# Optimization experiments

Hardware: AMD Instinct MI355X
Metric: run time of the kernel (lower is better)

## Reference

```python
import jax, jax.numpy as jnp
import numpy as np

N_NODES, N_EDGES, D, H, G = 50000, 800000, 128, 128, 2048
EPS_BN = 1e-5


def _bn(x, g, b, m, v):
    # inference-mode BatchNorm1d
    return (x - m) * jax.lax.rsqrt(v + EPS_BN) * g + b


def _gin_mlp(h, w1, b1, g1, be1, m1, v1, w2, b2, g2, be2, m2, v2):
    h = jax.nn.relu(_bn(h @ w1 + b1, g1, be1, m1, v1))
    return jax.nn.relu(_bn(h @ w2 + b2, g2, be2, m2, v2))


def _gin(x, src, dst, *mlp_params):
    # GINConv with eps=0: MLP(x_i + sum_{j->i} x_j)
    agg = jax.ops.segment_sum(x[src], dst, num_segments=x.shape[0])
    return _gin_mlp(x + agg, *mlp_params)


def setup_inputs() -> dict:
    key = jax.random.key(0)
    ks = jax.random.split(key, 16)
    inp = {
        'x': jax.random.normal(ks[0], (N_NODES, D), dtype=jnp.float32),
        'edge_index': jax.random.randint(ks[1], (2, N_EDGES), 0, N_NODES, dtype=jnp.int64),
        'batch': jnp.sort(jax.random.randint(ks[2], (N_NODES,), 0, G, dtype=jnp.int64)),
    }
    def lin(k, fin, fout):
        return jax.random.normal(k, (fin, fout), dtype=jnp.float32) * (1.0 / np.sqrt(fin))
    # conv1 MLP
    inp.update(w11=lin(ks[3], D, H), b11=jnp.zeros((H,)), g11=jnp.ones((H,)), be11=jnp.zeros((H,)), m11=jnp.zeros((H,)), v11=jnp.ones((H,)))
    inp.update(w12=lin(ks[4], H, H), b12=jnp.zeros((H,)), g12=jnp.ones((H,)), be12=jnp.zeros((H,)), m12=jnp.zeros((H,)), v12=jnp.ones((H,)))
    # conv2 MLP
    inp.update(w21=lin(ks[5], H, H), b21=jnp.zeros((H,)), g21=jnp.ones((H,)), be21=jnp.zeros((H,)), m21=jnp.zeros((H,)), v21=jnp.ones((H,)))
    inp.update(w22=lin(ks[6], H, H), b22=jnp.zeros((H,)), g22=jnp.ones((H,)), be22=jnp.zeros((H,)), m22=jnp.zeros((H,)), v22=jnp.ones((H,)))
    # classifier
    inp.update(wc1=lin(ks[7], H, 64), bc1=jnp.zeros((64,)), gc1=jnp.ones((64,)), bec1=jnp.zeros((64,)), mc1=jnp.zeros((64,)), vc1=jnp.ones((64,)))
    inp.update(wc2=lin(ks[8], 64, 2), bc2=jnp.zeros((2,)))
    return inp


def reference(x, edge_index, batch,
              w11, b11, g11, be11, m11, v11, w12, b12, g12, be12, m12, v12,
              w21, b21, g21, be21, m21, v21, w22, b22, g22, be22, m22, v22,
              wc1, bc1, gc1, bec1, mc1, vc1, wc2, bc2):
    src, dst = edge_index[0], edge_index[1]
    out1 = _gin(x, src, dst, w11, b11, g11, be11, m11, v11, w12, b12, g12, be12, m12, v12)
    # F.relu on already-ReLU'd output is a no-op but kept for fidelity
    out1 = jax.nn.relu(out1)
    out2 = _gin(out1, src, dst, w21, b21, g21, be21, m21, v21, w22, b22, g22, be22, m22, v22)
    out2 = jax.nn.relu(out2)
    # global mean pool over graph ids
    sums = jax.ops.segment_sum(out2, batch, num_segments=G)
    cnt = jax.ops.segment_sum(jnp.ones((out2.shape[0],), out2.dtype), batch, num_segments=G)
    pooled = sums / jnp.maximum(cnt, 1.0)[:, None]
    # classifier (dropout = identity in eval)
    h = jax.nn.relu(_bn(pooled @ wc1 + bc1, gc1, bec1, mc1, vc1))
    logits = h @ wc2 + bc2
    return logits
```

## Files before the change

kernel.cpp:

```cpp
#include <hip/hip_runtime.h>

#define NN 50000
#define NE 800000
#define DD 128
#define GG 2048
#define EPS 1e-5f
#define NBUK 196
#define CHUNK 4096
#define CAP 5120
#define CVTB 3125

typedef __attribute__((ext_vector_type(8))) short short8;
typedef __attribute__((ext_vector_type(4))) float floatx4;

__device__ __forceinline__ ushort f2b(float f) {
  uint u = __float_as_uint(f);
  uint r = ((u >> 16) & 1u) + 0x7fffu;
  return (ushort)((u + r) >> 16);
}
__device__ __forceinline__ float b2f(ushort h) {
  return __uint_as_float(((uint)h) << 16);
}
__device__ __forceinline__ float blo(uint u) { return __uint_as_float(u << 16); }
__device__ __forceinline__ float bhi(uint u) { return __uint_as_float(u & 0xffff0000u); }

__global__ __launch_bounds__(256) void k_pre(
    const float* __restrict__ W11, const float* __restrict__ W12,
    const float* __restrict__ W21, const float* __restrict__ W22,
    const float* __restrict__ b11, const float* __restrict__ g11,
    const float* __restrict__ be11, const float* __restrict__ m11,
    const float* __restrict__ v11,
    const float* __restrict__ b12, const float* __restrict__ g12,
    const float* __restrict__ be12, const float* __restrict__ m12,
    const float* __restrict__ v12,
    const float* __restrict__ b21, const float* __restrict__ g21,
    const float* __restrict__ be21, const float* __restrict__ m21,
    const float* __restrict__ v21,
    const float* __restrict__ b22, const float* __restrict__ g22,
    const float* __restrict__ be22, const float* __restrict__ m22,
    const float* __restrict__ v22,
    ushort* __restrict__ Wb, float* __restrict__ albb,
    int* __restrict__ buk_cnt) {
  int t = threadIdx.x;
  int b = blockIdx.x;
  if (b == 64) {
    buk_cnt[t] = 0;
    if (t < DD) {
      float a;
      a = g11[t] * rsqrtf(v11[t] + EPS);
      albb[0 * DD + t] = a;
      albb[1 * DD + t] = (b11[t] - m11[t]) * a + be11[t];
      a = g12[t] * rsqrtf(v12[t] + EPS);
      albb[2 * DD + t] = a;
      albb[3 * DD + t] = (b12[t] - m12[t]) * a + be12[t];
      a = g21[t] * rsqrtf(v21[t] + EPS);
      albb[4 * DD + t] = a;
      albb[5 * DD + t] = (b21[t] - m21[t]) * a + be21[t];
      a = g22[t] * rsqrtf(v22[t] + EPS);
      albb[6 * DD + t] = a;
      albb[7 * DD + t] = (b22[t] - m22[t]) * a + be22[t];
    }
    return;
  }
  const float* Ws[4] = {W11, W12, W21, W22};
  int widx = b >> 4;
  int idx = (b & 15) * 256 + t;
  int c = idx >> 5;
  int k0 = (idx & 31) * 4;
  const float* W = Ws[widx];
  ushort4 p;
  p.x = f2b(W[(k0 + 0) * DD + c]);
  p.y = f2b(W[(k0 + 1) * DD + c]);
  p.z = f2b(W[(k0 + 2) * DD + c]);
  p.w = f2b(W[(k0 + 3) * DD + c]);
  *(ushort4*)&Wb[(size_t)widx * DD * DD + c * DD + (k0 ^ ((c & 7) << 3))] = p;
}

__global__ __launch_bounds__(256) void k_binC(const float4* __restrict__ x,
                                              short8* __restrict__ xb,
                                              const int* __restrict__ ei,
                                              int* __restrict__ buk_cnt,
                                              uint* __restrict__ buk_pairs) {
  __shared__ int hist[256];
  __shared__ int gbase[256];
  __shared__ int lcur[256];
  int t = threadIdx.x;
  if (blockIdx.x < CVTB) {
    int i = blockIdx.x * 256 + t;
    float4 a = x[2 * i], c = x[2 * i + 1];
    short8 v;
    v[0] = (short)f2b(a.x); v[1] = (short)f2b(a.y);
    v[2] = (short)f2b(a.z); v[3] = (short)f2b(a.w);
    v[4] = (short)f2b(c.x); v[5] = (short)f2b(c.y);
    v[6] = (short)f2b(c.z); v[7] = (short)f2b(c.w);
    xb[i] = v;
    return;
  }
  int blk = blockIdx.x - CVTB;
  int e0 = blk * CHUNK;
  int nE = min(CHUNK, NE - e0);
  hist[t] = 0;
  lcur[t] = 0;
  gbase[t] = 0;
  __syncthreads();
  uint pk[16];
#pragma unroll
  for (int i = 0; i < 16; ++i) {
    int off = i * 256 + t;
    if (off < nE) {
      int e = e0 + off;
      int s = ei[e], d = ei[NE + e];
      int b = d >> 8;
      pk[i] = ((uint)b << 24) | ((uint)(d & 255) << 16) | (uint)s;
      atomicAdd(&hist[b], 1);
    } else {
      pk[i] = 0xffffffffu;
    }
  }
  __syncthreads();
  if (t < NBUK && hist[t] > 0) gbase[t] = atomicAdd(&buk_cnt[t], hist[t]);
  __syncthreads();
#pragma unroll
  for (int i = 0; i < 16; ++i) {
    if (pk[i] != 0xffffffffu) {
      int b = pk[i] >> 24;
      int lo = atomicAdd(&lcur[b], 1);
      int off = gbase[b] + lo;
      if (off < CAP) buk_pairs[(size_t)b * CAP + off] = pk[i];
    }
  }
}

__global__ __launch_bounds__(256) void k_bfill(const uint* __restrict__ buk_pairs,
                                               const int* __restrict__ buk_cnt,
                                               int* __restrict__ row_ptr,
                                               int* __restrict__ csr_src) {
  __shared__ int sc[256];
  __shared__ int deg[256];
  __shared__ int pos[256];
  int b = blockIdx.x, t = threadIdx.x;
  int c = (t < NBUK) ? min(buk_cnt[t], CAP) : 0;
  sc[t] = c;
  __syncthreads();
  int s1 = c;
  for (int off = 1; off < 256; off <<= 1) {
    int o = (t >= off) ? sc[t - off] : 0;
    __syncthreads();
    s1 += o;
    sc[t] = s1;
    __syncthreads();
  }
  int beg = (b == 0) ? 0 : sc[b - 1];
  int cnt = sc[b] - beg;
  const uint* src = buk_pairs + (size_t)b * CAP;
  deg[t] = 0;
  __syncthreads();
  for (int i = t; i < cnt; i += 256) {
    atomicAdd(&deg[(src[i] >> 16) & 255], 1);
  }
  __syncthreads();
  int d = deg[t];
  int sum = d;
  pos[t] = sum;
  __syncthreads();
  for (int off = 1; off < 256; off <<= 1) {
    int o = (t >= off) ? pos[t - off] : 0;
    __syncthreads();
    sum += o;
    pos[t] = sum;
    __syncthreads();
  }
  int myStart = beg + sum - d;
  int node = b * 256 + t;
  if (node < NN) row_ptr[node] = myStart;
  if (node == NN - 1) row_ptr[NN] = NE;
  __syncthreads();
  pos[t] = myStart;
  __syncthreads();
  for (int i = t; i < cnt; i += 256) {
    uint p = src[i];
    int lo = atomicAdd(&pos[(p >> 16) & 255], 1);
    csr_src[lo] = (int)(p & 0xffffu);
  }
}

__global__ __launch_bounds__(256) void k_agg(const uint* __restrict__ X,
                                             const int* __restrict__ row_ptr,
                                             const int* __restrict__ csr_src,
                                             uint* __restrict__ out) {
  int wid = (blockIdx.x * 256 + threadIdx.x) >> 6;
  int l = threadIdx.x & 63;
  int g = l >> 5, sl = l & 31;
  int node = wid * 2 + g;
  if (node >= NN) return;
  int base = g * 32;
  const uint2* Xr = (const uint2*)(X + (size_t)node * 64);
  uint2 s0 = Xr[sl];
  float a0 = blo(s0.x), a1 = bhi(s0.x), a2 = blo(s0.y), a3 = bhi(s0.y);
  int beg = row_ptr[node], end = row_ptr[node + 1];
  for (int i = beg; i < end; i += 32) {
    int idx = i + sl;
    int my = (idx < end) ? __builtin_nontemporal_load(csr_src + idx) : 0;
    int cnt = min(32, end - i);
    int j = 0;
    for (; j + 8 <= cnt; j += 8) {
      int n0 = __shfl(my, base + j + 0);
      int n1 = __shfl(my, base + j + 1);
      int n2 = __shfl(my, base + j + 2);
      int n3 = __shfl(my, base + j + 3);
      int n4 = __shfl(my, base + j + 4);
      int n5 = __shfl(my, base + j + 5);
      int n6 = __shfl(my, base + j + 6);
      int n7 = __shfl(my, base + j + 7);
      uint2 v0 = *(const uint2*)(X + (size_t)n0 * 64 + sl * 2);
      uint2 v1 = *(const uint2*)(X + (size_t)n1 * 64 + sl * 2);
      uint2 v2 = *(const uint2*)(X + (size_t)n2 * 64 + sl * 2);
      uint2 v3 = *(const uint2*)(X + (size_t)n3 * 64 + sl * 2);
      uint2 v4 = *(const uint2*)(X + (size_t)n4 * 64 + sl * 2);
      uint2 v5 = *(const uint2*)(X + (size_t)n5 * 64 + sl * 2);
      uint2 v6 = *(const uint2*)(X + (size_t)n6 * 64 + sl * 2);
      uint2 v7 = *(const uint2*)(X + (size_t)n7 * 64 + sl * 2);
      a0 += blo(v0.x); a1 += bhi(v0.x); a2 += blo(v0.y); a3 += bhi(v0.y);
      a0 += blo(v1.x); a1 += bhi(v1.x); a2 += blo(v1.y); a3 += bhi(v1.y);
      a0 += blo(v2.x); a1 += bhi(v2.x); a2 += blo(v2.y); a3 += bhi(v2.y);
      a0 += blo(v3.x); a1 += bhi(v3.x); a2 += blo(v3.y); a3 += bhi(v3.y);
      a0 += blo(v4.x); a1 += bhi(v4.x); a2 += blo(v4.y); a3 += bhi(v4.y);
      a0 += blo(v5.x); a1 += bhi(v5.x); a2 += blo(v5.y); a3 += bhi(v5.y);
      a0 += blo(v6.x); a1 += bhi(v6.x); a2 += blo(v6.y); a3 += bhi(v6.y);
      a0 += blo(v7.x); a1 += bhi(v7.x); a2 += blo(v7.y); a3 += bhi(v7.y);
    }
    for (; j + 4 <= cnt; j += 4) {
      int n0 = __shfl(my, base + j + 0);
      int n1 = __shfl(my, base + j + 1);
      int n2 = __shfl(my, base + j + 2);
      int n3 = __shfl(my, base + j + 3);
      uint2 v0 = *(const uint2*)(X + (size_t)n0 * 64 + sl * 2);
      uint2 v1 = *(const uint2*)(X + (size_t)n1 * 64 + sl * 2);
      uint2 v2 = *(const uint2*)(X + (size_t)n2 * 64 + sl * 2);
      uint2 v3 = *(const uint2*)(X + (size_t)n3 * 64 + sl * 2);
      a0 += blo(v0.x); a1 += bhi(v0.x); a2 += blo(v0.y); a3 += bhi(v0.y);
      a0 += blo(v1.x); a1 += bhi(v1.x); a2 += blo(v1.y); a3 += bhi(v1.y);
      a0 += blo(v2.x); a1 += bhi(v2.x); a2 += blo(v2.y); a3 += bhi(v2.y);
      a0 += blo(v3.x); a1 += bhi(v3.x); a2 += blo(v3.y); a3 += bhi(v3.y);
    }
    for (; j < cnt; ++j) {
      int s = __shfl(my, base + j);
      uint2 v = *(const uint2*)(X + (size_t)s * 64 + sl * 2);
      a0 += blo(v.x); a1 += bhi(v.x); a2 += blo(v.y); a3 += bhi(v.y);
    }
  }
  uint2 o;
  o.x = (uint)f2b(a0) | ((uint)f2b(a1) << 16);
  o.y = (uint)f2b(a2) | ((uint)f2b(a3) << 16);
  *(uint2*)(out + (size_t)node * 64 + sl * 2) = o;
}

__global__ __launch_bounds__(256) void k_mlp(const ushort* __restrict__ A,
                                             const ushort* __restrict__ Wb1,
                                             const ushort* __restrict__ Wb2,
                                             const float* __restrict__ albb,
                                             ushort* __restrict__ out) {
  __shared__ ushort Wt[DD * DD];
  __shared__ ushort mid[64 * DD];
  __shared__ float al1[DD], bb1[DD], al2[DD], bb2[DD];
  int t = threadIdx.x;
  for (int ii = t; ii < 2048; ii += 256) ((short8*)Wt)[ii] = ((const short8*)Wb1)[ii];
  if (t < DD) {
    al1[t] = albb[0 * DD + t];
    bb1[t] = albb[1 * DD + t];
    al2[t] = albb[2 * DD + t];
    bb2[t] = albb[3 * DD + t];
  }
  int w = t >> 6, l = t & 63;
  int lr = l & 15, lg = l >> 4;
  int rowBase = blockIdx.x * 64 + w * 16;
  int arow = min(rowBase + lr, NN - 1);
  const short8* Ar = (const short8*)(A + (size_t)arow * DD);
  short8 a0 = Ar[0 * 4 + lg];
  short8 a1 = Ar[1 * 4 + lg];
  short8 a2 = Ar[2 * 4 + lg];
  short8 a3 = Ar[3 * 4 + lg];
  __syncthreads();

  int mrowb = w * 16;
#pragma unroll
  for (int ct = 0; ct < 8; ++ct) {
    int c = ct * 16 + lr;
    int sw = (c & 7) << 3;
    const ushort* wr = Wt + c * DD;
    short8 b0 = *(const short8*)(wr + ((0 * 32 + lg * 8) ^ sw));
    short8 b1 = *(const short8*)(wr + ((1 * 32 + lg * 8) ^ sw));
    short8 b2 = *(const short8*)(wr + ((2 * 32 + lg * 8) ^ sw));
    short8 b3 = *(const short8*)(wr + ((3 * 32 + lg * 8) ^ sw));
    floatx4 acc = {0.f, 0.f, 0.f, 0.f};
    acc = __builtin_amdgcn_mfma_f32_16x16x32_bf16(a0, b0, acc, 0, 0, 0);
    acc = __builtin_amdgcn_mfma_f32_16x16x32_bf16(a1, b1, acc, 0, 0, 0);
    acc = __builtin_amdgcn_mfma_f32_16x16x32_bf16(a2, b2, acc, 0, 0, 0);
    acc = __builtin_amdgcn_mfma_f32_16x16x32_bf16(a3, b3, acc, 0, 0, 0);
    float alc = al1[c], bbc = bb1[c];
#pragma unroll
    for (int reg = 0; reg < 4; ++reg) {
      int row = mrowb + lg * 4 + reg;
      mid[row * DD + (c ^ ((row & 7) << 3))] = f2b(fmaxf(acc[reg] * alc + bbc, 0.f));
    }
  }
  __syncthreads();

  int mr = mrowb + lr;
  int msw = (mr & 7) << 3;
  const ushort* mrp = mid + mr * DD;
  short8 c0 = *(const short8*)(mrp + ((0 * 32 + lg * 8) ^ msw));
  short8 c1 = *(const short8*)(mrp + ((1 * 32 + lg * 8) ^ msw));
  short8 c2 = *(const short8*)(mrp + ((2 * 32 + lg * 8) ^ msw));
  short8 c3 = *(const short8*)(mrp + ((3 * 32 + lg * 8) ^ msw));
  for (int ii = t; ii < 2048; ii += 256) ((short8*)Wt)[ii] = ((const short8*)Wb2)[ii];
  __syncthreads();

#pragma unroll
  for (int ct = 0; ct < 8; ++ct) {
    int c = ct * 16 + lr;
    int sw = (c & 7) << 3;
    const ushort* wr = Wt + c * DD;
    short8 b0 = *(const short8*)(wr + ((0 * 32 + lg * 8) ^ sw));
    short8 b1 = *(const short8*)(wr + ((1 * 32 + lg * 8) ^ sw));
    short8 b2 = *(const short8*)(wr + ((2 * 32 + lg * 8) ^ sw));
    short8 b3 = *(const short8*)(wr + ((3 * 32 + lg * 8) ^ sw));
    floatx4 acc = {0.f, 0.f, 0.f, 0.f};
    acc = __builtin_amdgcn_mfma_f32_16x16x32_bf16(c0, b0, acc, 0, 0, 0);
    acc = __builtin_amdgcn_mfma_f32_16x16x32_bf16(c1, b1, acc, 0, 0, 0);
    acc = __builtin_amdgcn_mfma_f32_16x16x32_bf16(c2, b2, acc, 0, 0, 0);
    acc = __builtin_amdgcn_mfma_f32_16x16x32_bf16(c3, b3, acc, 0, 0, 0);
    float alc = al2[c], bbc = bb2[c];
#pragma unroll
    for (int reg = 0; reg < 4; ++reg) {
      int r = rowBase + lg * 4 + reg;
      if (r < NN) {
        out[(size_t)r * DD + c] = f2b(fmaxf(acc[reg] * alc + bbc, 0.f));
      }
    }
  }
}

__device__ __forceinline__ int lb(const int* __restrict__ a, int n, int v) {
  int lo = 0, hi = n;
  while (lo < hi) {
    int mid = (lo + hi) >> 1;
    if (a[mid] < v) lo = mid + 1;
    else hi = mid;
  }
  return lo;
}

__global__ __launch_bounds__(256) void k_poolcls(const ushort* __restrict__ h,
                                                 const int* __restrict__ batch,
                                                 const float* __restrict__ wc1,
                                                 const float* __restrict__ bc1,
                                                 const float* __restrict__ gc1,
                                                 const float* __restrict__ bec1,
                                                 const float* __restrict__ mc1,
                                                 const float* __restrict__ vc1,
                                                 const float* __restrict__ wc2,
                                                 const float* __restrict__ bc2,
                                                 float* __restrict__ outp) {
  __shared__ int sb[2];
  __shared__ float ps[DD];
  __shared__ float ps2[DD];
  __shared__ float hh[64];
  int g = blockIdx.x, t = threadIdx.x;
  if (t < 2) sb[t] = lb(batch, NN, g + t);
  __syncthreads();
  int beg = sb[0], end = sb[1];
  int c = t & 127;
  int half = t >> 7;
  int m = (beg + end) >> 1;
  int lo0 = half ? m : beg;
  int hi0 = half ? end : m;
  float acc = 0.f;
  int n = lo0;
  for (; n + 4 <= hi0; n += 4) {
    float x0 = b2f(h[(size_t)(n + 0) * DD + c]);
    float x1 = b2f(h[(size_t)(n + 1) * DD + c]);
    float x2 = b2f(h[(size_t)(n + 2) * DD + c]);
    float x3 = b2f(h[(size_t)(n + 3) * DD + c]);
    acc += x0 + x1 + x2 + x3;
  }
  for (; n < hi0; ++n) acc += b2f(h[(size_t)n * DD + c]);
  if (half) ps2[c] = acc;
  else ps[c] = acc;
  __syncthreads();
  if (t < DD) {
    float inv = 1.0f / fmaxf((float)(end - beg), 1.0f);
    ps[t] = (ps[t] + ps2[t]) * inv;
  }
  __syncthreads();
  if (t < 64) {
    float a2 = 0.f;
#pragma unroll 8
    for (int k = 0; k < DD; ++k) a2 += ps[k] * wc1[k * 64 + t];
    float a = gc1[t] * rsqrtf(vc1[t] + EPS);
    float b2 = (bc1[t] - mc1[t]) * a + bec1[t];
    hh[t] = fmaxf(a2 * a + b2, 0.f);
  }
  __syncthreads();
  if (t < 2) {
    float a2 = bc2[t];
#pragma unroll
    for (int k = 0; k < 64; ++k) a2 += hh[k] * wc2[k * 2 + t];
    outp[g * 2 + t] = a2;
  }
}

extern "C" void kernel_launch(void* const* d_in, const int* in_sizes, int n_in,
                              void* d_out, int out_size, void* d_ws, size_t ws_size,
                              hipStream_t stream) {
  const float* x = (const float*)d_in[0];
  const int* ei = (const int*)d_in[1];
  const int* batch = (const int*)d_in[2];
  const float* w11 = (const float*)d_in[3];
  const float* b11 = (const float*)d_in[4];
  const float* g11 = (const float*)d_in[5];
  const float* be11 = (const float*)d_in[6];
  const float* m11 = (const float*)d_in[7];
  const float* v11 = (const float*)d_in[8];
  const float* w12 = (const float*)d_in[9];
  const float* b12 = (const float*)d_in[10];
  const float* g12 = (const float*)d_in[11];
  const float* be12 = (const float*)d_in[12];
  const float* m12 = (const float*)d_in[13];
  const float* v12 = (const float*)d_in[14];
  const float* w21 = (const float*)d_in[15];
  const float* b21 = (const float*)d_in[16];
  const float* g21 = (const float*)d_in[17];
  const float* be21 = (const float*)d_in[18];
  const float* m21 = (const float*)d_in[19];
  const float* v21 = (const float*)d_in[20];
  const float* w22 = (const float*)d_in[21];
  const float* b22 = (const float*)d_in[22];
  const float* g22 = (const float*)d_in[23];
  const float* be22 = (const float*)d_in[24];
  const float* m22 = (const float*)d_in[25];
  const float* v22 = (const float*)d_in[26];
  const float* wc1 = (const float*)d_in[27];
  const float* bc1 = (const float*)d_in[28];
  const float* gc1 = (const float*)d_in[29];
  const float* bec1 = (const float*)d_in[30];
  const float* mc1 = (const float*)d_in[31];
  const float* vc1 = (const float*)d_in[32];
  const float* wc2 = (const float*)d_in[33];
  const float* bc2 = (const float*)d_in[34];

  const size_t NB = (size_t)NN * DD;
  ushort* XB = (ushort*)d_ws;
  ushort* AG = XB + NB;
  ushort* H1 = AG + NB;
  ushort* H2 = H1 + NB;
  int* row_ptr = (int*)(H2 + NB);
  int* buk_cnt = row_ptr + NN + 1;
  int* buk_base = buk_cnt + 256;
  int* csr_src = buk_base + 256;
  uint* buk_pairs = (uint*)(csr_src + NE);
  ushort* Wb = (ushort*)(buk_pairs + (size_t)NBUK * CAP);
  float* albb = (float*)(Wb + 4 * DD * DD);

  const int gemmBlocks = (NN + 63) / 64;
  const int aggBlocks = NN / 8;

  k_pre<<<65, 256, 0, stream>>>(w11, w12, w21, w22,
                                b11, g11, be11, m11, v11,
                                b12, g12, be12, m12, v12,
                                b21, g21, be21, m21, v21,
                                b22, g22, be22, m22, v22,
                                Wb, albb, buk_cnt);
  k_binC<<<CVTB + NBUK, 256, 0, stream>>>((const float4*)x, (short8*)XB, ei,
                                          buk_cnt, buk_pairs);
  k_bfill<<<NBUK, 256, 0, stream>>>(buk_pairs, buk_cnt, row_ptr, csr_src);

  k_agg<<<aggBlocks, 256, 0, stream>>>((const uint*)XB, row_ptr, csr_src, (uint*)AG);
  k_mlp<<<gemmBlocks, 256, 0, stream>>>(AG, Wb, Wb + DD * DD, albb, H1);

  k_agg<<<aggBlocks, 256, 0, stream>>>((const uint*)H1, row_ptr, csr_src, (uint*)AG);
  k_mlp<<<gemmBlocks, 256, 0, stream>>>(AG, Wb + 2 * DD * DD, Wb + 3 * DD * DD,
                                        albb + 4 * DD, H2);

  k_poolcls<<<GG, 256, 0, stream>>>(H2, batch, wc1, bc1, gc1, bec1, mc1, vc1,
                                    wc2, bc2, (float*)d_out);
}
```

Before: 150.4 us.

## Process two 64-row tiles per MLP block to reuse staged weights

```diff
diff --git a/kernel.cpp b/kernel.cpp
--- a/kernel.cpp
+++ b/kernel.cpp
@@ -273,16 +273,27 @@
   }
   int w = t >> 6, l = t & 63;
   int lr = l & 15, lg = l >> 4;
-  int rowBase = blockIdx.x * 64 + w * 16;
-  int arow = min(rowBase + lr, NN - 1);
-  const short8* Ar = (const short8*)(A + (size_t)arow * DD);
-  short8 a0 = Ar[0 * 4 + lg];
-  short8 a1 = Ar[1 * 4 + lg];
-  short8 a2 = Ar[2 * 4 + lg];
-  short8 a3 = Ar[3 * 4 + lg];
+  int rowA = blockIdx.x * 128 + w * 16;
+  int rowB = rowA + 64;
+  int arA = min(rowA + lr, NN - 1);
+  int arB = min(rowB + lr, NN - 1);
+  const short8* ArA = (const short8*)(A + (size_t)arA * DD);
+  const short8* ArB = (const short8*)(A + (size_t)arB * DD);
+  short8 aA0 = ArA[0 * 4 + lg];
+  short8 aA1 = ArA[1 * 4 + lg];
+  short8 aA2 = ArA[2 * 4 + lg];
+  short8 aA3 = ArA[3 * 4 + lg];
+  short8 aB0 = ArB[0 * 4 + lg];
+  short8 aB1 = ArB[1 * 4 + lg];
+  short8 aB2 = ArB[2 * 4 + lg];
+  short8 aB3 = ArB[3 * 4 + lg];
   __syncthreads();
 
   int mrowb = w * 16;
+  int mr = mrowb + lr;
+  int msw = (mr & 7) << 3;
+  const ushort* mrp = mid + mr * DD;
+
 #pragma unroll
   for (int ct = 0; ct < 8; ++ct) {
     int c = ct * 16 + lr;
@@ -293,10 +304,10 @@
     short8 b2 = *(const short8*)(wr + ((2 * 32 + lg * 8) ^ sw));
     short8 b3 = *(const short8*)(wr + ((3 * 32 + lg * 8) ^ sw));
     floatx4 acc = {0.f, 0.f, 0.f, 0.f};
-    acc = __builtin_amdgcn_mfma_f32_16x16x32_bf16(a0, b0, acc, 0, 0, 0);
-    acc = __builtin_amdgcn_mfma_f32_16x16x32_bf16(a1, b1, acc, 0, 0, 0);
-    acc = __builtin_amdgcn_mfma_f32_16x16x32_bf16(a2, b2, acc, 0, 0, 0);
-    acc = __builtin_amdgcn_mfma_f32_16x16x32_bf16(a3, b3, acc, 0, 0, 0);
+    acc = __builtin_amdgcn_mfma_f32_16x16x32_bf16(aA0, b0, acc, 0, 0, 0);
+    acc = __builtin_amdgcn_mfma_f32_16x16x32_bf16(aA1, b1, acc, 0, 0, 0);
+    acc = __builtin_amdgcn_mfma_f32_16x16x32_bf16(aA2, b2, acc, 0, 0, 0);
+    acc = __builtin_amdgcn_mfma_f32_16x16x32_bf16(aA3, b3, acc, 0, 0, 0);
     float alc = al1[c], bbc = bb1[c];
 #pragma unroll
     for (int reg = 0; reg < 4; ++reg) {
@@ -304,17 +315,10 @@
       mid[row * DD + (c ^ ((row & 7) << 3))] = f2b(fmaxf(acc[reg] * alc + bbc, 0.f));
     }
   }
-  __syncthreads();
-
-  int mr = mrowb + lr;
-  int msw = (mr & 7) << 3;
-  const ushort* mrp = mid + mr * DD;
-  short8 c0 = *(const short8*)(mrp + ((0 * 32 + lg * 8) ^ msw));
-  short8 c1 = *(const short8*)(mrp + ((1 * 32 + lg * 8) ^ msw));
-  short8 c2 = *(const short8*)(mrp + ((2 * 32 + lg * 8) ^ msw));
-  short8 c3 = *(const short8*)(mrp + ((3 * 32 + lg * 8) ^ msw));
-  for (int ii = t; ii < 2048; ii += 256) ((short8*)Wt)[ii] = ((const short8*)Wb2)[ii];
-  __syncthreads();
+  short8 cA0 = *(const short8*)(mrp + ((0 * 32 + lg * 8) ^ msw));
+  short8 cA1 = *(const short8*)(mrp + ((1 * 32 + lg * 8) ^ msw));
+  short8 cA2 = *(const short8*)(mrp + ((2 * 32 + lg * 8) ^ msw));
+  short8 cA3 = *(const short8*)(mrp + ((3 * 32 + lg * 8) ^ msw));
 
 #pragma unroll
   for (int ct = 0; ct < 8; ++ct) {
@@ -326,14 +330,67 @@
     short8 b2 = *(const short8*)(wr + ((2 * 32 + lg * 8) ^ sw));
     short8 b3 = *(const short8*)(wr + ((3 * 32 + lg * 8) ^ sw));
     floatx4 acc = {0.f, 0.f, 0.f, 0.f};
-    acc = __builtin_amdgcn_mfma_f32_16x16x32_bf16(c0, b0, acc, 0, 0, 0);
-    acc = __builtin_amdgcn_mfma_f32_16x16x32_bf16(c1, b1, acc, 0, 0, 0);
-    acc = __builtin_amdgcn_mfma_f32_16x16x32_bf16(c2, b2, acc, 0, 0, 0);
-    acc = __builtin_amdgcn_mfma_f32_16x16x32_bf16(c3, b3, acc, 0, 0, 0);
+    acc = __builtin_amdgcn_mfma_f32_16x16x32_bf16(aB0, b0, acc, 0, 0, 0);
+    acc = __builtin_amdgcn_mfma_f32_16x16x32_bf16(aB1, b1, acc, 0, 0, 0);
+    acc = __builtin_amdgcn_mfma_f32_16x16x32_bf16(aB2, b2, acc, 0, 0, 0);
+    acc = __builtin_amdgcn_mfma_f32_16x16x32_bf16(aB3, b3, acc, 0, 0, 0);
+    float alc = al1[c], bbc = bb1[c];
+#pragma unroll
+    for (int reg = 0; reg < 4; ++reg) {
+      int row = mrowb + lg * 4 + reg;
+      mid[row * DD + (c ^ ((row & 7) << 3))] = f2b(fmaxf(acc[reg] * alc + bbc, 0.f));
+    }
+  }
+  short8 cB0 = *(const short8*)(mrp + ((0 * 32 + lg * 8) ^ msw));
+  short8 cB1 = *(const short8*)(mrp + ((1 * 32 + lg * 8) ^ msw));
+  short8 cB2 = *(const short8*)(mrp + ((2 * 32 + lg * 8) ^ msw));
+  short8 cB3 = *(const short8*)(mrp + ((3 * 32 + lg * 8) ^ msw));
+
+  __syncthreads();
+  for (int ii = t; ii < 2048; ii += 256) ((short8*)Wt)[ii] = ((const short8*)Wb2)[ii];
+  __syncthreads();
+
+#pragma unroll
+  for (int ct = 0; ct < 8; ++ct) {
+    int c = ct * 16 + lr;
+    int sw = (c & 7) << 3;
+    const ushort* wr = Wt + c * DD;
+    short8 b0 = *(const short8*)(wr + ((0 * 32 + lg * 8) ^ sw));
+    short8 b1 = *(const short8*)(wr + ((1 * 32 + lg * 8) ^ sw));
+    short8 b2 = *(const short8*)(wr + ((2 * 32 + lg * 8) ^ sw));
+    short8 b3 = *(const short8*)(wr + ((3 * 32 + lg * 8) ^ sw));
+    floatx4 acc = {0.f, 0.f, 0.f, 0.f};
+    acc = __builtin_amdgcn_mfma_f32_16x16x32_bf16(cA0, b0, acc, 0, 0, 0);
+    acc = __builtin_amdgcn_mfma_f32_16x16x32_bf16(cA1, b1, acc, 0, 0, 0);
+    acc = __builtin_amdgcn_mfma_f32_16x16x32_bf16(cA2, b2, acc, 0, 0, 0);
+    acc = __builtin_amdgcn_mfma_f32_16x16x32_bf16(cA3, b3, acc, 0, 0, 0);
     float alc = al2[c], bbc = bb2[c];
 #pragma unroll
     for (int reg = 0; reg < 4; ++reg) {
-      int r = rowBase + lg * 4 + reg;
+      int r = rowA + lg * 4 + reg;
+      if (r < NN) {
+        out[(size_t)r * DD + c] = f2b(fmaxf(acc[reg] * alc + bbc, 0.f));
+      }
+    }
+  }
+#pragma unroll
+  for (int ct = 0; ct < 8; ++ct) {
+    int c = ct * 16 + lr;
+    int sw = (c & 7) << 3;
+    const ushort* wr = Wt + c * DD;
+    short8 b0 = *(const short8*)(wr + ((0 * 32 + lg * 8) ^ sw));
+    short8 b1 = *(const short8*)(wr + ((1 * 32 + lg * 8) ^ sw));
+    short8 b2 = *(const short8*)(wr + ((2 * 32 + lg * 8) ^ sw));
+    short8 b3 = *(const short8*)(wr + ((3 * 32 + lg * 8) ^ sw));
+    floatx4 acc = {0.f, 0.f, 0.f, 0.f};
+    acc = __builtin_amdgcn_mfma_f32_16x16x32_bf16(cB0, b0, acc, 0, 0, 0);
+    acc = __builtin_amdgcn_mfma_f32_16x16x32_bf16(cB1, b1, acc, 0, 0, 0);
+    acc = __builtin_amdgcn_mfma_f32_16x16x32_bf16(cB2, b2, acc, 0, 0, 0);
+    acc = __builtin_amdgcn_mfma_f32_16x16x32_bf16(cB3, b3, acc, 0, 0, 0);
+    float alc = al2[c], bbc = bb2[c];
+#pragma unroll
+    for (int reg = 0; reg < 4; ++reg) {
+      int r = rowB + lg * 4 + reg;
       if (r < NN) {
         out[(size_t)r * DD + c] = f2b(fmaxf(acc[reg] * alc + bbc, 0.f));
       }
@@ -462,7 +519,7 @@
   ushort* Wb = (ushort*)(buk_pairs + (size_t)NBUK * CAP);
   float* albb = (float*)(Wb + 4 * DD * DD);
 
-  const int gemmBlocks = (NN + 63) / 64;
+  const int gemmBlocks = (NN + 127) / 128;
   const int aggBlocks = NN / 8;
 
   k_pre<<<65, 256, 0, stream>>>(w11, w12, w21, w22,
```

After: 147.8 us. About the same (-1.8%).
